# Optimization experiments

Hardware: AMD Instinct MI355X
Metric: run time of the kernel (lower is better)

The kernel has to match this reference:

```python
import jax, jax.numpy as jnp
import numpy as np

VOCAB, EMB, H, LAYERS, B, T = 50000, 128, 128, 3, 64, 512


def _lstm_dir(x, w_ih, w_hh, b_ih, b_hh, h0, c0, reverse):
    # x: [B,T,Din]; w_ih: [4H,Din]; w_hh: [4H,H]; h0,c0: [B,H]
    xg = jnp.einsum('btd,gd->btg', x, w_ih) + b_ih + b_hh  # [B,T,4H]

    def step(carry, xg_t):
        h, c = carry
        g = xg_t + h @ w_hh.T  # [B,4H]
        i, f, gg, o = jnp.split(g, 4, axis=-1)  # torch gate order i,f,g,o
        c = jax.nn.sigmoid(f) * c + jax.nn.sigmoid(i) * jnp.tanh(gg)
        h = jax.nn.sigmoid(o) * jnp.tanh(c)
        return (h, c), h

    _, hs = jax.lax.scan(step, (h0, c0), jnp.swapaxes(xg, 0, 1), reverse=reverse)
    return jnp.swapaxes(hs, 0, 1)  # [B,T,H], aligned with input time order


def _bidir_layer(x, w_ih, w_hh, b_ih, b_hh, h0, c0):
    # stacked params: leading dim 2 = (fwd, bwd)
    fwd = _lstm_dir(x, w_ih[0], w_hh[0], b_ih[0], b_hh[0], h0[0], c0[0], False)
    bwd = _lstm_dir(x, w_ih[1], w_hh[1], b_ih[1], b_hh[1], h0[1], c0[1], True)
    return jnp.concatenate([fwd, bwd], axis=-1)  # [B,T,2H]


def setup_inputs() -> dict:
    key = jax.random.key(0)
    ks = jax.random.split(key, 20)
    s = 1.0 / np.sqrt(H)
    inp = {
        'X_batch': jax.random.randint(ks[0], (B, T), 0, VOCAB),
        'emb': jax.random.normal(ks[1], (VOCAB, EMB), jnp.float32),
        'hx': jax.random.normal(ks[2], (2 * LAYERS, B, H), jnp.float32),
        'cx': jax.random.normal(ks[3], (2 * LAYERS, B, H), jnp.float32),
        'lin_w': jax.random.uniform(ks[4], (1, 2 * H), jnp.float32, -s, s),
        'lin_b': jax.random.uniform(ks[5], (1,), jnp.float32, -s, s),
    }
    k = 6
    for l in range(LAYERS):
        din = EMB if l == 0 else 2 * H
        inp[f'w_ih_{l}'] = jax.random.uniform(ks[k], (2, 4 * H, din), jnp.float32, -s, s); k += 1
        inp[f'w_hh_{l}'] = jax.random.uniform(ks[k], (2, 4 * H, H), jnp.float32, -s, s); k += 1
        inp[f'b_ih_{l}'] = jax.random.uniform(ks[k], (2, 4 * H), jnp.float32, -s, s); k += 1
        inp[f'b_hh_{l}'] = jax.random.uniform(ks[k], (2, 4 * H), jnp.float32, -s, s); k += 1
    return inp


def reference(X_batch, emb, hx, cx, lin_w, lin_b,
              w_ih_0, w_hh_0, b_ih_0, b_hh_0,
              w_ih_1, w_hh_1, b_ih_1, b_hh_1,
              w_ih_2, w_hh_2, b_ih_2, b_hh_2):
    x = emb[X_batch]  # [B,T,EMB]
    params = [(w_ih_0, w_hh_0, b_ih_0, b_hh_0),
              (w_ih_1, w_hh_1, b_ih_1, b_hh_1),
              (w_ih_2, w_hh_2, b_ih_2, b_hh_2)]
    for l, (wi, wh, bi, bh) in enumerate(params):
        x = _bidir_layer(x, wi, wh, bi, bh, hx[2 * l:2 * l + 2], cx[2 * l:2 * l + 2])
    # linear head applied to last timestep (== output[:, -1] of full linear)
    return x[:, -1] @ lin_w.T + lin_b  # [B,1]
```

## Files before the change

### kernel.cpp

```cpp
#include <hip/hip_runtime.h>
#include <hip/hip_bf16.h>
#include <stdint.h>

#define B_    64
#define T_    512
#define EMB_  128
#define H_    128
#define G4    512
#define M_    (B_ * T_)

typedef __attribute__((ext_vector_type(8))) short     short8;
typedef __attribute__((ext_vector_type(4))) float     floatx4;
typedef __attribute__((ext_vector_type(2))) _Float16  half2v;

#define GLDS(g, l) __builtin_amdgcn_global_load_lds( \
    (__attribute__((address_space(1))) void*)(g),    \
    (__attribute__((address_space(3))) void*)(l), 16, 0, 0)

__device__ __forceinline__ unsigned short f2bf_bits(float f) {
  __hip_bfloat16 h = __float2bfloat16(f);
  return *reinterpret_cast<unsigned short*>(&h);
}
__device__ __forceinline__ float bf_bits2f(unsigned short u) {
  unsigned int x = ((unsigned int)u) << 16;
  return __uint_as_float(x);
}
__device__ __forceinline__ float sigm(float x) {
  return __fdividef(1.0f, 1.0f + __expf(-x));
}
__device__ __forceinline__ float tanh_fast(float x) {
  return 1.0f - __fdividef(2.0f, __expf(2.0f * x) + 1.0f);
}

__device__ __forceinline__ unsigned int pack_f16x2(float a, float b) {
  half2v h; h.x = (_Float16)a; h.y = (_Float16)b;
  return __builtin_bit_cast(unsigned int, h);
}
__device__ __forceinline__ half2v u2h2(unsigned int u) {
  return __builtin_bit_cast(half2v, u);
}

#if __has_builtin(__builtin_amdgcn_fdot2)
__device__ __forceinline__ float fdot2(half2v a, half2v b, float c) {
  return __builtin_amdgcn_fdot2(a, b, c, false);
}
#else
__device__ __forceinline__ float fdot2(half2v a, half2v b, float c) {
  return fmaf((float)a.x, (float)b.x, fmaf((float)a.y, (float)b.y, c));
}
#endif

__device__ __forceinline__ float pair_bfly_add(float x) {
  return x + __int_as_float(
      __builtin_amdgcn_mov_dpp(__float_as_int(x), 0xB1, 0xF, 0xF, true));
}

__device__ __forceinline__ void barrier_lds_only() {
  __builtin_amdgcn_s_waitcnt(0xC07F);
  __builtin_amdgcn_s_barrier();
}

__device__ __forceinline__ void  store_xg(float* p, float v)  { *p = v; }
__device__ __forceinline__ void  store_xg(unsigned short* p, float v) { *p = f2bf_bits(v); }
__device__ __forceinline__ float load_xg(const float* p)  { return *p; }
__device__ __forceinline__ float load_xg(const unsigned short* p) { return bf_bits2f(*p); }

__global__ void k_gather(const int* __restrict__ X, const float* __restrict__ emb,
                         unsigned short* __restrict__ x0) {
  int i = blockIdx.x * 256 + threadIdx.x;
  int row = i >> 5, c4 = i & 31;
  float4 v = ((const float4*)emb)[(size_t)X[row] * 32 + c4];
  ushort4 o;
  o.x = f2bf_bits(v.x); o.y = f2bf_bits(v.y); o.z = f2bf_bits(v.z); o.w = f2bf_bits(v.w);
  ((ushort4*)x0)[i] = o;
}

__global__ void k_prep(const float* __restrict__ w, const float* __restrict__ bi,
                       const float* __restrict__ bh, unsigned short* __restrict__ wb,
                       float* __restrict__ bias, int nw) {
  int i = blockIdx.x * blockDim.x + threadIdx.x;
  int stride = gridDim.x * blockDim.x;
  for (int k = i; k < nw; k += stride) wb[k] = f2bf_bits(w[k]);
  for (int k = i; k < 2 * G4; k += stride) bias[k] = bi[k] + bh[k];
}

__global__ void k_prep_whh(const float* __restrict__ Whh, unsigned int* __restrict__ wf) {
  int i = blockIdx.x * 256 + threadIdx.x;
  int dir = i >> 15;
  int r   = i & 0x7FFF;
  int i4  = r >> 10;
  int r2  = r & 0x3FF;
  int ts  = r2 >> 2;
  int q   = r2 & 3;
  int d   = i4 * 4 + q;
  int g   = d >> 5;
  int jj  = d & 31;
  int lane = ts & 63, w = ts >> 6;
  int p = lane & 1, ul = lane >> 1;
  int u = w * 32 + ul;
  int k = 64 * p + 2 * jj;
  const float* wr = Whh + ((size_t)dir * G4 + g * H_ + u) * H_ + k;
  wf[i] = pack_f16x2(wr[0], wr[1]);
}

template <typename XG_T>
__global__ __launch_bounds__(256, 2) void k_gemm(
    const unsigned short* __restrict__ A,
    const unsigned short* __restrict__ W,
    const float* __restrict__ bias,
    XG_T* __restrict__ xg,
    int K) {
  __shared__ unsigned short sA[128 * 32];
  __shared__ unsigned short sB[128 * 32];
  const int tid  = threadIdx.x;
  const int lane = tid & 63;
  const int wave = tid >> 6;
  const int mt = blockIdx.x, nt = blockIdx.y, dir = blockIdx.z;
  const size_t Arow0 = (size_t)mt * 128;
  const int    Ncol0 = nt * 128;
  const unsigned short* Wd = W + (size_t)dir * G4 * K;

  const int srow = tid >> 2;
  const int qlog = (tid & 3) ^ ((tid >> 4) & 3);
  auto ldsA0 = (__attribute__((address_space(3))) void*)(sA + wave * 512);
  auto ldsA1 = (__attribute__((address_space(3))) void*)(sA + 2048 + wave * 512);
  auto ldsB0 = (__attribute__((address_space(3))) void*)(sB + wave * 512);
  auto ldsB1 = (__attribute__((address_space(3))) void*)(sB + 2048 + wave * 512);

  floatx4 acc[4][4];
#pragma unroll
  for (int i = 0; i < 4; ++i)
#pragma unroll
    for (int j = 0; j < 4; ++j) acc[i][j] = (floatx4)0.0f;

  const int wrow = (wave >> 1) * 64, wcol = (wave & 1) * 64;
  const int frow = lane & 15;
  const int fq   = lane >> 4;

  for (int kt = 0; kt < K; kt += 32) {
    const unsigned short* gA0 = A  + (Arow0 + srow) * (size_t)K + kt + qlog * 8;
    const unsigned short* gB0 = Wd + (size_t)(Ncol0 + srow) * K + kt + qlog * 8;
    GLDS(gA0, ldsA0);
    GLDS(gA0 + (size_t)64 * K, ldsA1);
    GLDS(gB0, ldsB0);
    GLDS(gB0 + (size_t)64 * K, ldsB1);
    __syncthreads();

    short8 af[4], bf[4];
#pragma unroll
    for (int i = 0; i < 4; ++i) {
      int r  = wrow + 16 * i + frow;
      int rn = wcol + 16 * i + frow;
      af[i] = *(const short8*)(sA + r  * 32 + ((fq ^ ((r  >> 2) & 3)) * 8));
      bf[i] = *(const short8*)(sB + rn * 32 + ((fq ^ ((rn >> 2) & 3)) * 8));
    }
#pragma unroll
    for (int i = 0; i < 4; ++i)
#pragma unroll
      for (int j = 0; j < 4; ++j)
        acc[i][j] = __builtin_amdgcn_mfma_f32_16x16x32_bf16(af[i], bf[j], acc[i][j], 0, 0, 0);
    __syncthreads();
  }

  const int r0 = (lane >> 4) * 4;
  const int cc = lane & 15;
  XG_T* xgd = xg + (size_t)dir * M_ * G4;
#pragma unroll
  for (int j = 0; j < 4; ++j) {
    int gcol = Ncol0 + wcol + 16 * j + cc;
    float bs = bias[dir * G4 + gcol];
#pragma unroll
    for (int i = 0; i < 4; ++i) {
      size_t rowb = Arow0 + wrow + 16 * i + r0;
#pragma unroll
      for (int r = 0; r < 4; ++r)
        store_xg(&xgd[(rowb + r) * G4 + gcol], acc[i][j][r] + bs);
    }
  }
}

template <typename XG_T>
__global__ __attribute__((amdgpu_flat_work_group_size(256, 256),
                          amdgpu_waves_per_eu(1, 1))) void k_scan(
    const unsigned int* __restrict__ wf,
    const float* __restrict__ hx0,
    const float* __restrict__ cx0,
    const XG_T* __restrict__ xg,
    unsigned short* __restrict__ y)
{
  const int b   = blockIdx.x & 63;
  const int dir = blockIdx.x >> 6;
  const int tid = threadIdx.x;
  const int lane = tid & 63;
  const int wave = tid >> 6;
  const int p  = lane & 1;
  const int ul = lane >> 1;
  const int u  = wave * 32 + ul;

  __shared__ __align__(16) unsigned short h16[2][128];

  uint4 wv[32];
  const uint4* wfv = (const uint4*)wf;
#pragma unroll
  for (int i = 0; i < 32; ++i) wv[i] = wfv[(dir * 32 + i) * 256 + tid];

  float c = cx0[(size_t)dir * B_ * H_ + b * H_ + u];
  if (p == 0) {
    float h0 = hx0[(size_t)dir * B_ * H_ + b * H_ + u];
    h16[0][u] = (unsigned short)(pack_f16x2(h0, 0.0f) & 0xFFFF);
  }

  const XG_T* xgb = xg + ((size_t)dir * M_ + (size_t)b * T_) * G4;
  const intptr_t xstep = dir ? -(intptr_t)G4 : (intptr_t)G4;
  const int o0 = (2 * p) * H_ + u;
  const int o1 = o0 + H_;
  const XG_T* xrow0 = xgb + (dir ? (size_t)(T_ - 1) * G4 : 0);
  float xa0 = load_xg(xrow0 + o0), xb0 = load_xg(xrow0 + o1);
  float xa1 = load_xg(xrow0 + xstep + o0), xb1 = load_xg(xrow0 + xstep + o1);
  const XG_T* xld = xrow0 + 2 * xstep;

  unsigned short* yp = y + ((size_t)b * T_ + (dir ? T_ - 1 : 0)) * (2 * H_)
                         + dir * H_ + u;
  const intptr_t ystep = dir ? -(intptr_t)(2 * H_) : (intptr_t)(2 * H_);

  __syncthreads();

  auto dots = [&](int par, float xva, float xvb,
                  float& g0, float& g1, float& g2, float& g3) {
    const uint4* hv4 = (const uint4*)&h16[par][0];
    uint4 hq[8];
#pragma unroll
    for (int i = 0; i < 8; ++i) hq[i] = hv4[8 * p + i];
    half2v hh[32];
#pragma unroll
    for (int i = 0; i < 8; ++i) {
      hh[4 * i + 0] = u2h2(hq[i].x);
      hh[4 * i + 1] = u2h2(hq[i].y);
      hh[4 * i + 2] = u2h2(hq[i].z);
      hh[4 * i + 3] = u2h2(hq[i].w);
    }
    float A0 = 0, B0 = 0, A1 = 0, B1 = 0, A2 = 0, B2 = 0, A3 = 0, B3 = 0;
#pragma unroll
    for (int j = 0; j < 16; ++j) {
      int d0 = j, d1 = j + 16;
      A0 = fdot2(u2h2(((const unsigned int*)&wv[(0 * 32 + d0) >> 2])[(0 * 32 + d0) & 3]), hh[d0], A0);
      A1 = fdot2(u2h2(((const unsigned int*)&wv[(1 * 32 + d0) >> 2])[(1 * 32 + d0) & 3]), hh[d0], A1);
      A2 = fdot2(u2h2(((const unsigned int*)&wv[(2 * 32 + d0) >> 2])[(2 * 32 + d0) & 3]), hh[d0], A2);
      A3 = fdot2(u2h2(((const unsigned int*)&wv[(3 * 32 + d0) >> 2])[(3 * 32 + d0) & 3]), hh[d0], A3);
      B0 = fdot2(u2h2(((const unsigned int*)&wv[(0 * 32 + d1) >> 2])[(0 * 32 + d1) & 3]), hh[d1], B0);
      B1 = fdot2(u2h2(((const unsigned int*)&wv[(1 * 32 + d1) >> 2])[(1 * 32 + d1) & 3]), hh[d1], B1);
      B2 = fdot2(u2h2(((const unsigned int*)&wv[(2 * 32 + d1) >> 2])[(2 * 32 + d1) & 3]), hh[d1], B2);
      B3 = fdot2(u2h2(((const unsigned int*)&wv[(3 * 32 + d1) >> 2])[(3 * 32 + d1) & 3]), hh[d1], B3);
    }
    g0 = A0 + B0; g1 = A1 + B1; g2 = A2 + B2; g3 = A3 + B3;
    g0 += (p == 0) ? xva : 0.0f;
    g1 += (p == 0) ? xvb : 0.0f;
    g2 += (p == 1) ? xva : 0.0f;
    g3 += (p == 1) ? xvb : 0.0f;
  };

  auto finish = [&](int par, float g0, float g1, float g2, float g3) {
    g0 = pair_bfly_add(g0);
    g1 = pair_bfly_add(g1);
    g2 = pair_bfly_add(g2);
    g3 = pair_bfly_add(g3);
    float iv = sigm(g0), fv = sigm(g1), gv = tanh_fast(g2), ov = sigm(g3);
    c = fmaf(fv, c, iv * gv);
    float h = ov * tanh_fast(c);
    if (p == 0) {
      h16[par ^ 1][u] = (unsigned short)(pack_f16x2(h, 0.0f) & 0xFFFF);
      *yp = f2bf_bits(h);
    }
    yp += ystep;
    barrier_lds_only();
  };

  for (int t = 0; t < T_; t += 2) {
    {
      float va = xa0, vb = xb0;
      if (t + 2 < T_) { xa0 = load_xg(xld + o0); xb0 = load_xg(xld + o1); }
      else            { xa0 = 0.0f; xb0 = 0.0f; }
      xld += xstep;
      float a0, a1, a2, a3;
      dots(0, va, vb, a0, a1, a2, a3);
      finish(0, a0, a1, a2, a3);
    }
    {
      float va = xa1, vb = xb1;
      if (t + 3 < T_) { xa1 = load_xg(xld + o0); xb1 = load_xg(xld + o1); }
      else            { xa1 = 0.0f; xb1 = 0.0f; }
      xld += xstep;
      float a0, a1, a2, a3;
      dots(1, va, vb, a0, a1, a2, a3);
      finish(1, a0, a1, a2, a3);
    }
  }
}

__global__ void k_head(const unsigned short* __restrict__ y2, const float* __restrict__ lw,
                       const float* __restrict__ lb, float* __restrict__ out) {
  int b = blockIdx.x, l = threadIdx.x;
  const unsigned short* row = y2 + ((size_t)b * T_ + (T_ - 1)) * (2 * H_);
  float s = 0;
#pragma unroll
  for (int k = 0; k < 4; ++k) s += bf_bits2f(row[l + 64 * k]) * lw[l + 64 * k];
#pragma unroll
  for (int off = 32; off > 0; off >>= 1) s += __shfl_down(s, off);
  if (l == 0) out[b] = s + lb[0];
}

template <typename XG_T>
static inline void run_layers(const unsigned int* const* wfs,
                              const unsigned short* x0,
                              unsigned short* y0, unsigned short* y1, unsigned short* y2,
                              const unsigned short* wb0, const unsigned short* wb1,
                              const unsigned short* wb2,
                              const float* bias0, const float* bias1, const float* bias2,
                              const float* hx, const float* cx,
                              XG_T* xg, hipStream_t stream) {
  dim3 gg(M_ / 128, G4 / 128, 2);
  k_gemm<XG_T><<<gg, 256, 0, stream>>>(x0, wb0, bias0, xg, EMB_);
  k_scan<XG_T><<<128, 256, 0, stream>>>(wfs[0], hx, cx, xg, y0);
  k_gemm<XG_T><<<gg, 256, 0, stream>>>(y0, wb1, bias1, xg, 2 * H_);
  k_scan<XG_T><<<128, 256, 0, stream>>>(wfs[1], hx + 2 * B_ * H_, cx + 2 * B_ * H_, xg, y1);
  k_gemm<XG_T><<<gg, 256, 0, stream>>>(y1, wb2, bias2, xg, 2 * H_);
  k_scan<XG_T><<<128, 256, 0, stream>>>(wfs[2], hx + 4 * B_ * H_, cx + 4 * B_ * H_, xg, y2);
}

extern "C" void kernel_launch(void* const* d_in, const int* in_sizes, int n_in,
                              void* d_out, int out_size, void* d_ws, size_t ws_size,
                              hipStream_t stream) {
  const int*   X   = (const int*)d_in[0];
  const float* emb = (const float*)d_in[1];
  const float* hx  = (const float*)d_in[2];
  const float* cx  = (const float*)d_in[3];
  const float* lw  = (const float*)d_in[4];
  const float* lb  = (const float*)d_in[5];
  const float* w_ih[3] = {(const float*)d_in[6],  (const float*)d_in[10], (const float*)d_in[14]};
  const float* w_hh[3] = {(const float*)d_in[7],  (const float*)d_in[11], (const float*)d_in[15]};
  const float* b_ih[3] = {(const float*)d_in[8],  (const float*)d_in[12], (const float*)d_in[16]};
  const float* b_hh[3] = {(const float*)d_in[9],  (const float*)d_in[13], (const float*)d_in[17]};
  float* out = (float*)d_out;

  char* ws = (char*)d_ws;
  size_t off = 0;
  auto carve = [&](size_t bytes) {
    char* p = ws + off;
    off = (off + bytes + 255) & ~(size_t)255;
    return p;
  };
  unsigned short* x0  = (unsigned short*)carve((size_t)M_ * EMB_ * 2);
  unsigned short* y0  = (unsigned short*)carve((size_t)M_ * 2 * H_ * 2);
  unsigned short* y1  = (unsigned short*)carve((size_t)M_ * 2 * H_ * 2);
  unsigned short* y2  = (unsigned short*)carve((size_t)M_ * 2 * H_ * 2);
  unsigned short* wb0 = (unsigned short*)carve((size_t)2 * G4 * EMB_ * 2);
  unsigned short* wb1 = (unsigned short*)carve((size_t)2 * G4 * 2 * H_ * 2);
  unsigned short* wb2 = (unsigned short*)carve((size_t)2 * G4 * 2 * H_ * 2);
  float* bias0 = (float*)carve(2 * G4 * 4);
  float* bias1 = (float*)carve(2 * G4 * 4);
  float* bias2 = (float*)carve(2 * G4 * 4);
  unsigned int* wf0 = (unsigned int*)carve((size_t)65536 * 4);
  unsigned int* wf1 = (unsigned int*)carve((size_t)65536 * 4);
  unsigned int* wf2 = (unsigned int*)carve((size_t)65536 * 4);
  const size_t xg_f32_bytes = (size_t)2 * M_ * G4 * 4;
  const bool use_f32 = (off + xg_f32_bytes) <= ws_size;
  void* xg = carve(use_f32 ? xg_f32_bytes : xg_f32_bytes / 2);

  k_prep<<<256, 256, 0, stream>>>(w_ih[0], b_ih[0], b_hh[0], wb0, bias0, 2 * G4 * EMB_);
  k_prep<<<256, 256, 0, stream>>>(w_ih[1], b_ih[1], b_hh[1], wb1, bias1, 2 * G4 * 2 * H_);
  k_prep<<<256, 256, 0, stream>>>(w_ih[2], b_ih[2], b_hh[2], wb2, bias2, 2 * G4 * 2 * H_);
  k_prep_whh<<<256, 256, 0, stream>>>(w_hh[0], wf0);
  k_prep_whh<<<256, 256, 0, stream>>>(w_hh[1], wf1);
  k_prep_whh<<<256, 256, 0, stream>>>(w_hh[2], wf2);
  k_gather<<<(M_ * 32) / 256, 256, 0, stream>>>(X, emb, x0);

  const unsigned int* wfs[3] = {wf0, wf1, wf2};
  if (use_f32)
    run_layers<float>(wfs, x0, y0, y1, y2, wb0, wb1, wb2, bias0, bias1, bias2,
                      hx, cx, (float*)xg, stream);
  else
    run_layers<unsigned short>(wfs, x0, y0, y1, y2, wb0, wb1, wb2, bias0, bias1, bias2,
                               hx, cx, (unsigned short*)xg, stream);

  k_head<<<64, 64, 0, stream>>>(y2, lw, lb, out);
}
```

Before: 1.121 ms.

## Process two batch rows per scan block, sharing register-resident weights

Each scan block now advances two independent batch sequences in lockstep, reusing the register-held recurrent weights for both dot-product sets and issuing one LDS barrier per step instead of one per sequence. The grid shrinks from 128 to 64 blocks. The aim is to hide the latency of each sequential step with independent work and to halve the barrier count per element. In exchange each step has twice the ALU work per block, and fewer CUs are occupied on a 256-CU part, so the serial critical path per step grows.

```diff
diff --git a/kernel.cpp b/kernel.cpp
--- a/kernel.cpp
+++ b/kernel.cpp
@@ -188,8 +188,9 @@
     const XG_T* __restrict__ xg,
     unsigned short* __restrict__ y)
 {
-  const int b   = blockIdx.x & 63;
-  const int dir = blockIdx.x >> 6;
+  const int bA  = blockIdx.x & 31;
+  const int bB  = bA + 32;
+  const int dir = blockIdx.x >> 5;
   const int tid = threadIdx.x;
   const int lane = tid & 63;
   const int wave = tid >> 6;
@@ -197,37 +198,47 @@
   const int ul = lane >> 1;
   const int u  = wave * 32 + ul;
 
-  __shared__ __align__(16) unsigned short h16[2][128];
+  __shared__ __align__(16) unsigned short h16[2][2][128];
 
   uint4 wv[32];
   const uint4* wfv = (const uint4*)wf;
 #pragma unroll
   for (int i = 0; i < 32; ++i) wv[i] = wfv[(dir * 32 + i) * 256 + tid];
 
-  float c = cx0[(size_t)dir * B_ * H_ + b * H_ + u];
+  float cA = cx0[(size_t)dir * B_ * H_ + bA * H_ + u];
+  float cB = cx0[(size_t)dir * B_ * H_ + bB * H_ + u];
   if (p == 0) {
-    float h0 = hx0[(size_t)dir * B_ * H_ + b * H_ + u];
-    h16[0][u] = (unsigned short)(pack_f16x2(h0, 0.0f) & 0xFFFF);
+    h16[0][0][u] = (unsigned short)(pack_f16x2(
+        hx0[(size_t)dir * B_ * H_ + bA * H_ + u], 0.0f) & 0xFFFF);
+    h16[0][1][u] = (unsigned short)(pack_f16x2(
+        hx0[(size_t)dir * B_ * H_ + bB * H_ + u], 0.0f) & 0xFFFF);
   }
 
-  const XG_T* xgb = xg + ((size_t)dir * M_ + (size_t)b * T_) * G4;
   const intptr_t xstep = dir ? -(intptr_t)G4 : (intptr_t)G4;
   const int o0 = (2 * p) * H_ + u;
   const int o1 = o0 + H_;
-  const XG_T* xrow0 = xgb + (dir ? (size_t)(T_ - 1) * G4 : 0);
-  float xa0 = load_xg(xrow0 + o0), xb0 = load_xg(xrow0 + o1);
-  float xa1 = load_xg(xrow0 + xstep + o0), xb1 = load_xg(xrow0 + xstep + o1);
-  const XG_T* xld = xrow0 + 2 * xstep;
-
-  unsigned short* yp = y + ((size_t)b * T_ + (dir ? T_ - 1 : 0)) * (2 * H_)
-                         + dir * H_ + u;
+  const XG_T* xrowA = xg + ((size_t)dir * M_ + (size_t)bA * T_) * G4
+                        + (dir ? (size_t)(T_ - 1) * G4 : 0);
+  const XG_T* xrowB = xg + ((size_t)dir * M_ + (size_t)bB * T_) * G4
+                        + (dir ? (size_t)(T_ - 1) * G4 : 0);
+  float xa0A = load_xg(xrowA + o0), xb0A = load_xg(xrowA + o1);
+  float xa1A = load_xg(xrowA + xstep + o0), xb1A = load_xg(xrowA + xstep + o1);
+  float xa0B = load_xg(xrowB + o0), xb0B = load_xg(xrowB + o1);
+  float xa1B = load_xg(xrowB + xstep + o0), xb1B = load_xg(xrowB + xstep + o1);
+  const XG_T* xldA = xrowA + 2 * xstep;
+  const XG_T* xldB = xrowB + 2 * xstep;
+
+  unsigned short* ypA = y + ((size_t)bA * T_ + (dir ? T_ - 1 : 0)) * (2 * H_)
+                          + dir * H_ + u;
+  unsigned short* ypB = y + ((size_t)bB * T_ + (dir ? T_ - 1 : 0)) * (2 * H_)
+                          + dir * H_ + u;
   const intptr_t ystep = dir ? -(intptr_t)(2 * H_) : (intptr_t)(2 * H_);
 
   __syncthreads();
 
-  auto dots = [&](int par, float xva, float xvb,
+  auto dots = [&](int par, int s, float xva, float xvb,
                   float& g0, float& g1, float& g2, float& g3) {
-    const uint4* hv4 = (const uint4*)&h16[par][0];
+    const uint4* hv4 = (const uint4*)&h16[par][s][0];
     uint4 hq[8];
 #pragma unroll
     for (int i = 0; i < 8; ++i) hq[i] = hv4[8 * p + i];
@@ -259,7 +270,8 @@
     g3 += (p == 1) ? xvb : 0.0f;
   };
 
-  auto finish = [&](int par, float g0, float g1, float g2, float g3) {
+  auto finish = [&](int par, int s, float& c, unsigned short*& yp,
+                    float g0, float g1, float g2, float g3) {
     g0 = pair_bfly_add(g0);
     g1 = pair_bfly_add(g1);
     g2 = pair_bfly_add(g2);
@@ -268,31 +280,40 @@
     c = fmaf(fv, c, iv * gv);
     float h = ov * tanh_fast(c);
     if (p == 0) {
-      h16[par ^ 1][u] = (unsigned short)(pack_f16x2(h, 0.0f) & 0xFFFF);
+      h16[par ^ 1][s][u] = (unsigned short)(pack_f16x2(h, 0.0f) & 0xFFFF);
       *yp = f2bf_bits(h);
     }
     yp += ystep;
-    barrier_lds_only();
   };
 
   for (int t = 0; t < T_; t += 2) {
     {
-      float va = xa0, vb = xb0;
-      if (t + 2 < T_) { xa0 = load_xg(xld + o0); xb0 = load_xg(xld + o1); }
-      else            { xa0 = 0.0f; xb0 = 0.0f; }
-      xld += xstep;
-      float a0, a1, a2, a3;
-      dots(0, va, vb, a0, a1, a2, a3);
-      finish(0, a0, a1, a2, a3);
+      float vaA = xa0A, vbA = xb0A, vaB = xa0B, vbB = xb0B;
+      if (t + 2 < T_) {
+        xa0A = load_xg(xldA + o0); xb0A = load_xg(xldA + o1);
+        xa0B = load_xg(xldB + o0); xb0B = load_xg(xldB + o1);
+      } else { xa0A = xb0A = xa0B = xb0B = 0.0f; }
+      xldA += xstep; xldB += xstep;
+      float a0, a1, a2, a3, b0, b1, b2, b3;
+      dots(0, 0, vaA, vbA, a0, a1, a2, a3);
+      dots(0, 1, vaB, vbB, b0, b1, b2, b3);
+      finish(0, 0, cA, ypA, a0, a1, a2, a3);
+      finish(0, 1, cB, ypB, b0, b1, b2, b3);
+      barrier_lds_only();
     }
     {
-      float va = xa1, vb = xb1;
-      if (t + 3 < T_) { xa1 = load_xg(xld + o0); xb1 = load_xg(xld + o1); }
-      else            { xa1 = 0.0f; xb1 = 0.0f; }
-      xld += xstep;
-      float a0, a1, a2, a3;
-      dots(1, va, vb, a0, a1, a2, a3);
-      finish(1, a0, a1, a2, a3);
+      float vaA = xa1A, vbA = xb1A, vaB = xa1B, vbB = xb1B;
+      if (t + 3 < T_) {
+        xa1A = load_xg(xldA + o0); xb1A = load_xg(xldA + o1);
+        xa1B = load_xg(xldB + o0); xb1B = load_xg(xldB + o1);
+      } else { xa1A = xb1A = xa1B = xb1B = 0.0f; }
+      xldA += xstep; xldB += xstep;
+      float a0, a1, a2, a3, b0, b1, b2, b3;
+      dots(1, 0, vaA, vbA, a0, a1, a2, a3);
+      dots(1, 1, vaB, vbB, b0, b1, b2, b3);
+      finish(1, 0, cA, ypA, a0, a1, a2, a3);
+      finish(1, 1, cB, ypB, b0, b1, b2, b3);
+      barrier_lds_only();
     }
   }
 }
@@ -320,11 +341,11 @@
                               XG_T* xg, hipStream_t stream) {
   dim3 gg(M_ / 128, G4 / 128, 2);
   k_gemm<XG_T><<<gg, 256, 0, stream>>>(x0, wb0, bias0, xg, EMB_);
-  k_scan<XG_T><<<128, 256, 0, stream>>>(wfs[0], hx, cx, xg, y0);
+  k_scan<XG_T><<<64, 256, 0, stream>>>(wfs[0], hx, cx, xg, y0);
   k_gemm<XG_T><<<gg, 256, 0, stream>>>(y0, wb1, bias1, xg, 2 * H_);
-  k_scan<XG_T><<<128, 256, 0, stream>>>(wfs[1], hx + 2 * B_ * H_, cx + 2 * B_ * H_, xg, y1);
+  k_scan<XG_T><<<64, 256, 0, stream>>>(wfs[1], hx + 2 * B_ * H_, cx + 2 * B_ * H_, xg, y1);
   k_gemm<XG_T><<<gg, 256, 0, stream>>>(y1, wb2, bias2, xg, 2 * H_);
-  k_scan<XG_T><<<128, 256, 0, stream>>>(wfs[2], hx + 4 * B_ * H_, cx + 4 * B_ * H_, xg, y2);
+  k_scan<XG_T><<<64, 256, 0, stream>>>(wfs[2], hx + 4 * B_ * H_, cx + 4 * B_ * H_, xg, y2);
 }
 
 extern "C" void kernel_launch(void* const* d_in, const int* in_sizes, int n_in,
```

After: 1.911 ms. 1.7x slower.
